# Kernel tuning notes

Hardware: AMD Instinct MI355X
Metric: run time of the kernel (lower is better)

Reference implementation:

```python
import jax, jax.numpy as jnp
import numpy as np

B, C, W, H = 32, 128, 128, 128  # batch, channels, window_size, prediction_horizon
KAPPA = 10.0

def setup_inputs() -> dict:
    key = jax.random.key(0)
    k1, k2, k3, k4 = jax.random.split(key, 4)
    x_t = jax.random.normal(k1, (B, C, W), dtype=jnp.float32)
    # d are observation timestamps in [0, H), compared against ref_t = linspace(0, H, H)
    d = jax.random.uniform(k2, (B, C, W), dtype=jnp.float32) * H
    # m is an observation mask/weight in (0, 1]; avoid exact zeros for log(m)
    m = jax.random.uniform(k3, (B, C, W), dtype=jnp.float32, minval=1e-3, maxval=1.0)
    kernel = jax.random.normal(k4, (W,), dtype=jnp.float32) * 0.1
    return {"x_t": x_t, "d": d, "m": m, "kernel": kernel}

def reference(x_t, d, m, kernel):
    # ref_t: [H], matches torch.linspace(0, H, H)
    ref_t = jnp.linspace(0.0, H, H, dtype=x_t.dtype)
    # norm: [B,C,W,H] squared time differences
    norm = (d[..., None] - ref_t) ** 2
    alpha = jnp.log1p(jnp.exp(kernel))[None, None, :, None]  # softplus, [1,1,W,1]
    logm = jnp.log(m)[..., None]                             # [B,C,W,1]
    # low-intensity interpolation (softmax over window dim W)
    s = -alpha * norm + logm                                 # [B,C,W,H]
    w = jax.nn.logsumexp(s, axis=2)                          # [B,C,H]
    w1 = jnp.exp(s - w[:, :, None, :])                       # softmax weights
    y = jnp.einsum('bcwh,bcw->bch', w1, x_t)
    # high-intensity (transient) interpolation with sharper kernel kappa*alpha
    s_t = -KAPPA * alpha * norm + logm
    wt_lse = jax.nn.logsumexp(s_t, axis=2)
    w_t = jnp.exp(s_t - wt_lse[:, :, None, :])
    y_trans = jnp.einsum('bcwh,bcw->bch', w_t, x_t)
    return (y, w, y_trans)
```

## Files before the change

### kernel.cpp

```cpp
#include <hip/hip_runtime.h>
#include <hip/hip_bf16.h>

#define NB 32
#define NC 128
#define NW 128
#define NH 128
#define BCH (NB * NC * NH)

__global__ __launch_bounds__(128, 4) void sci_kernel(
    const void* __restrict__ xp, const void* __restrict__ dp,
    const void* __restrict__ mp, const void* __restrict__ kp,
    void* __restrict__ outp)
{
    const int bc   = blockIdx.x;
    const int tid  = threadIdx.x;
    const int lane = tid & 63;
    const int wid  = tid >> 6;

    __shared__ float4 tileS[NW];
    __shared__ int    cum[NW + 1];
    __shared__ int    wtot[2];
    __shared__ float  wmin[2];

    const unsigned short* du16 = (const unsigned short*)dp;
    bool is_bf16 = true;
    #pragma unroll
    for (int i = 0; i < 32; i += 2) {
        float v = __uint_as_float(((unsigned int)du16[i]) << 16);
        is_bf16 = is_bf16 && (v >= 0.0f) && (v <= 129.0f);
    }

    float dv, mv, xv, kv;
    {
        const int base = bc * NW + tid;
        if (is_bf16) {
            dv = __bfloat162float(((const __hip_bfloat16*)dp)[base]);
            mv = __bfloat162float(((const __hip_bfloat16*)mp)[base]);
            xv = __bfloat162float(((const __hip_bfloat16*)xp)[base]);
            kv = __bfloat162float(((const __hip_bfloat16*)kp)[tid]);
        } else {
            dv = ((const float*)dp)[base];
            mv = ((const float*)mp)[base];
            xv = ((const float*)xp)[base];
            kv = ((const float*)kp)[tid];
        }
    }
    const float LOG2E = 1.4426950408889634f;
    float ex  = __builtin_amdgcn_exp2f(kv * LOG2E);
    float A2  = __builtin_amdgcn_logf(1.0f + ex);
    float sA2 = sqrtf(A2);
    float sd  = sA2 * dv;

    float rmn = sA2;
    #pragma unroll
    for (int o = 32; o >= 1; o >>= 1) rmn = fminf(rmn, __shfl_xor(rmn, o));
    if (lane == 0) wmin[wid] = rmn;

    cum[tid] = 0;
    __syncthreads();
    int bin  = min(127, max(0, (int)dv));
    int slot = atomicAdd(&cum[bin], 1);
    __syncthreads();

    int cnt = cum[tid];
    int c = cnt;
    #pragma unroll
    for (int o = 1; o < 64; o <<= 1) {
        int n = __shfl_up(c, o);
        if (lane >= o) c += n;
    }
    if (lane == 63) wtot[wid] = c;
    __syncthreads();
    int excl = c - cnt + (wid ? wtot[0] : 0);
    cum[tid] = excl;
    if (tid == 0) cum[NW] = NW;
    __syncthreads();

    int pos = cum[bin] + slot;
    tileS[pos] = make_float4(sA2, sd, mv, mv * xv);
    __syncthreads();

    const float rsA2min = (1.0f / fminf(wmin[0], wmin[1])) * 1.0005f;

    const float rh = (float)tid * (128.0f / 127.0f);

    float mn = 1e30f;
    float s1 = 0.f, a1 = 0.f, s2 = 0.f, a2 = 0.f;

    auto body = [&](int k) {
        float4 q = tileS[k];
        float t  = __builtin_fmaf(-q.x, rh, q.y);
        float t2 = t * t;
        if (t2 < mn) {
            float f  = __builtin_amdgcn_exp2f(t2 - mn);
            float fs = f * f, f4 = fs * fs, f8 = f4 * f4;
            float f10 = f8 * fs;
            s1 *= f; a1 *= f; s2 *= f10; a2 *= f10;
            mn = t2;
        }
        float g1 = __builtin_amdgcn_exp2f(mn - t2);
        float sq = g1 * g1, p4 = sq * sq, p8 = p4 * p4;
        float g2 = p8 * sq;
        s1 = __builtin_fmaf(q.z, g1, s1);
        a1 = __builtin_fmaf(q.w, g1, a1);
        s2 = __builtin_fmaf(q.z, g2, s2);
        a2 = __builtin_fmaf(q.w, g2, a2);
    };

    int b0 = min(127, (int)rh);
    int lo0, hi0, s0, e0;
    {
        int r = 2;
        for (;;) {
            lo0 = max(0, b0 - r); hi0 = min(127, b0 + r);
            s0 = cum[lo0]; e0 = cum[hi0 + 1];
            if (s0 != e0) break;
            ++r;
        }
    }
    for (int k = s0; k < e0; ++k) body(k);

    float Rh = sqrtf(mn + 12.0f) * rsA2min;
    int lo = min(lo0, max(0, (int)(rh - Rh)));
    int hi = max(hi0, min(127, (int)(rh + Rh)));
    int ks = cum[lo], ke = cum[hi + 1];
    for (int k = ks; k < s0; ++k) body(k);
    for (int k = e0; k < ke; ++k) body(k);

    const float LN2 = 0.6931471805599453f;
    float y  = a1 * __builtin_amdgcn_rcpf(s1);
    float wo = (__builtin_amdgcn_logf(s1) - mn) * LN2;
    float yt = a2 * __builtin_amdgcn_rcpf(s2);

    const int o = bc * NH + tid;
    if (is_bf16) {
        __hip_bfloat16* o16 = (__hip_bfloat16*)outp;
        o16[o]           = __float2bfloat16(y);
        o16[BCH + o]     = __float2bfloat16(wo);
        o16[2 * BCH + o] = __float2bfloat16(yt);
    } else {
        float* o32 = (float*)outp;
        o32[o]           = y;
        o32[BCH + o]     = wo;
        o32[2 * BCH + o] = yt;
    }
}

extern "C" void kernel_launch(void* const* d_in, const int* in_sizes, int n_in,
                              void* d_out, int out_size, void* d_ws, size_t ws_size,
                              hipStream_t stream) {
    const void* x_t = d_in[0];
    const void* d   = d_in[1];
    const void* m   = d_in[2];
    const void* k   = d_in[3];
    dim3 grid(NB * NC);
    dim3 block(128);
    hipLaunchKernelGGL(sci_kernel, grid, block, 0, stream, x_t, d, m, k, d_out);
}
```

Baseline: 72.89 us.

## Map one wavefront per (b,c) row with two outputs per lane

```diff
diff --git a/kernel.cpp b/kernel.cpp
--- a/kernel.cpp
+++ b/kernel.cpp
@@ -6,21 +6,31 @@
 #define NW 128
 #define NH 128
 #define BCH (NB * NC * NH)
+#define CPB 4
 
-__global__ __launch_bounds__(128, 4) void sci_kernel(
+#define WAVE_SYNC() do { __builtin_amdgcn_wave_barrier(); \
+    asm volatile("s_waitcnt lgkmcnt(0)" ::: "memory"); } while (0)
+
+static __device__ __forceinline__ float b2f(unsigned short u) {
+    return __uint_as_float(((unsigned int)u) << 16);
+}
+static __device__ __forceinline__ unsigned short f2b(float f) {
+    __hip_bfloat16 h = __float2bfloat16(f);
+    return *reinterpret_cast<unsigned short*>(&h);
+}
+
+__global__ __launch_bounds__(256, 4) void sci_kernel(
     const void* __restrict__ xp, const void* __restrict__ dp,
     const void* __restrict__ mp, const void* __restrict__ kp,
     void* __restrict__ outp)
 {
-    const int bc   = blockIdx.x;
-    const int tid  = threadIdx.x;
-    const int lane = tid & 63;
-    const int wid  = tid >> 6;
+    const int wid  = threadIdx.x >> 6;
+    const int lane = threadIdx.x & 63;
+    const int bc   = blockIdx.x * CPB + wid;
 
-    __shared__ float4 tileS[NW];
-    __shared__ int    cum[NW + 1];
-    __shared__ int    wtot[2];
-    __shared__ float  wmin[2];
+    __shared__ int    cnt[CPB][NW];
+    __shared__ int    cum[CPB][NW + 1];
+    __shared__ float4 tile[CPB][NW];
 
     const unsigned short* du16 = (const unsigned short*)dp;
     bool is_bf16 = true;
@@ -30,119 +40,141 @@
         is_bf16 = is_bf16 && (v >= 0.0f) && (v <= 129.0f);
     }
 
-    float dv, mv, xv, kv;
-    {
-        const int base = bc * NW + tid;
-        if (is_bf16) {
-            dv = __bfloat162float(((const __hip_bfloat16*)dp)[base]);
-            mv = __bfloat162float(((const __hip_bfloat16*)mp)[base]);
-            xv = __bfloat162float(((const __hip_bfloat16*)xp)[base]);
-            kv = __bfloat162float(((const __hip_bfloat16*)kp)[tid]);
-        } else {
-            dv = ((const float*)dp)[base];
-            mv = ((const float*)mp)[base];
-            xv = ((const float*)xp)[base];
-            kv = ((const float*)kp)[tid];
-        }
+    const int w0   = lane * 2;
+    const int base = bc * NW + w0;
+    float dv0, mv0, xv0, kv0, dv1, mv1, xv1, kv1;
+    if (is_bf16) {
+        ushort2 dd = *(const ushort2*)((const unsigned short*)dp + base);
+        ushort2 mm = *(const ushort2*)((const unsigned short*)mp + base);
+        ushort2 xx = *(const ushort2*)((const unsigned short*)xp + base);
+        ushort2 kk = *(const ushort2*)((const unsigned short*)kp + w0);
+        dv0 = b2f(dd.x); dv1 = b2f(dd.y);
+        mv0 = b2f(mm.x); mv1 = b2f(mm.y);
+        xv0 = b2f(xx.x); xv1 = b2f(xx.y);
+        kv0 = b2f(kk.x); kv1 = b2f(kk.y);
+    } else {
+        float2 dd = *(const float2*)((const float*)dp + base);
+        float2 mm = *(const float2*)((const float*)mp + base);
+        float2 xx = *(const float2*)((const float*)xp + base);
+        float2 kk = *(const float2*)((const float*)kp + w0);
+        dv0 = dd.x; dv1 = dd.y; mv0 = mm.x; mv1 = mm.y;
+        xv0 = xx.x; xv1 = xx.y; kv0 = kk.x; kv1 = kk.y;
     }
+
     const float LOG2E = 1.4426950408889634f;
-    float ex  = __builtin_amdgcn_exp2f(kv * LOG2E);
-    float A2  = __builtin_amdgcn_logf(1.0f + ex);
-    float sA2 = sqrtf(A2);
-    float sd  = sA2 * dv;
+    float ex0 = __builtin_amdgcn_exp2f(kv0 * LOG2E);
+    float ex1 = __builtin_amdgcn_exp2f(kv1 * LOG2E);
+    float A20 = __builtin_amdgcn_logf(1.0f + ex0);
+    float A21 = __builtin_amdgcn_logf(1.0f + ex1);
+    float sA20 = sqrtf(A20), sA21 = sqrtf(A21);
 
-    float rmn = sA2;
+    float rmn = fminf(sA20, sA21);
     #pragma unroll
     for (int o = 32; o >= 1; o >>= 1) rmn = fminf(rmn, __shfl_xor(rmn, o));
-    if (lane == 0) wmin[wid] = rmn;
+    const float rs = 1.0005f / rmn;
 
-    cum[tid] = 0;
-    __syncthreads();
-    int bin  = min(127, max(0, (int)dv));
-    int slot = atomicAdd(&cum[bin], 1);
-    __syncthreads();
-
-    int cnt = cum[tid];
-    int c = cnt;
+    cnt[wid][w0] = 0; cnt[wid][w0 + 1] = 0;
+    WAVE_SYNC();
+    int b0i = min(127, max(0, (int)dv0));
+    int b1i = min(127, max(0, (int)dv1));
+    int s0i = atomicAdd(&cnt[wid][b0i], 1);
+    int s1i = atomicAdd(&cnt[wid][b1i], 1);
+    WAVE_SYNC();
+    int c0 = cnt[wid][w0], c1 = cnt[wid][w0 + 1];
+    int p = c0 + c1, P = p;
     #pragma unroll
     for (int o = 1; o < 64; o <<= 1) {
-        int n = __shfl_up(c, o);
-        if (lane >= o) c += n;
+        int n = __shfl_up(P, o);
+        if (lane >= o) P += n;
     }
-    if (lane == 63) wtot[wid] = c;
-    __syncthreads();
-    int excl = c - cnt + (wid ? wtot[0] : 0);
-    cum[tid] = excl;
-    if (tid == 0) cum[NW] = NW;
-    __syncthreads();
+    int E0 = P - p;
+    cum[wid][w0]     = E0;
+    cum[wid][w0 + 1] = E0 + c0;
+    if (lane == 63) cum[wid][NW] = NW;
+    WAVE_SYNC();
+    int pos0 = cum[wid][b0i] + s0i;
+    int pos1 = cum[wid][b1i] + s1i;
+    tile[wid][pos0] = make_float4(sA20, sA20 * dv0, mv0, mv0 * xv0);
+    tile[wid][pos1] = make_float4(sA21, sA21 * dv1, mv1, mv1 * xv1);
+    WAVE_SYNC();
 
-    int pos = cum[bin] + slot;
-    tileS[pos] = make_float4(sA2, sd, mv, mv * xv);
-    __syncthreads();
+    const float STEP = 128.0f / 127.0f;
+    const float rh0 = (float)w0 * STEP;
+    const float rh1 = rh0 + STEP;
 
-    const float rsA2min = (1.0f / fminf(wmin[0], wmin[1])) * 1.0005f;
+    float mn0 = 1e30f, s10 = 0.f, a10 = 0.f, s20 = 0.f, a20 = 0.f;
+    float mn1 = 1e30f, s11 = 0.f, a11 = 0.f, s21 = 0.f, a21 = 0.f;
 
-    const float rh = (float)tid * (128.0f / 127.0f);
-
-    float mn = 1e30f;
-    float s1 = 0.f, a1 = 0.f, s2 = 0.f, a2 = 0.f;
+    const float4* T  = tile[wid];
+    const int*    CU = cum[wid];
 
     auto body = [&](int k) {
-        float4 q = tileS[k];
-        float t  = __builtin_fmaf(-q.x, rh, q.y);
-        float t2 = t * t;
-        if (t2 < mn) {
-            float f  = __builtin_amdgcn_exp2f(t2 - mn);
-            float fs = f * f, f4 = fs * fs, f8 = f4 * f4;
-            float f10 = f8 * fs;
-            s1 *= f; a1 *= f; s2 *= f10; a2 *= f10;
-            mn = t2;
+        float4 q = T[k];
+        float t0 = __builtin_fmaf(-q.x, rh0, q.y);
+        float t1 = __builtin_fmaf(-q.x, rh1, q.y);
+        float u0 = t0 * t0, u1 = t1 * t1;
+        if (u0 < mn0) {
+            float f = __builtin_amdgcn_exp2f(u0 - mn0);
+            float fs = f * f, f4 = fs * fs, f8 = f4 * f4, f10 = f8 * fs;
+            s10 *= f; a10 *= f; s20 *= f10; a20 *= f10; mn0 = u0;
         }
-        float g1 = __builtin_amdgcn_exp2f(mn - t2);
-        float sq = g1 * g1, p4 = sq * sq, p8 = p4 * p4;
-        float g2 = p8 * sq;
-        s1 = __builtin_fmaf(q.z, g1, s1);
-        a1 = __builtin_fmaf(q.w, g1, a1);
-        s2 = __builtin_fmaf(q.z, g2, s2);
-        a2 = __builtin_fmaf(q.w, g2, a2);
+        if (u1 < mn1) {
+            float f = __builtin_amdgcn_exp2f(u1 - mn1);
+            float fs = f * f, f4 = fs * fs, f8 = f4 * f4, f10 = f8 * fs;
+            s11 *= f; a11 *= f; s21 *= f10; a21 *= f10; mn1 = u1;
+        }
+        float g0 = __builtin_amdgcn_exp2f(mn0 - u0);
+        float g1 = __builtin_amdgcn_exp2f(mn1 - u1);
+        float q0 = g0 * g0, p40 = q0 * q0, p80 = p40 * p40, G0 = p80 * q0;
+        float q1 = g1 * g1, p41 = q1 * q1, p81 = p41 * p41, G1 = p81 * q1;
+        s10 = __builtin_fmaf(q.z, g0, s10); a10 = __builtin_fmaf(q.w, g0, a10);
+        s20 = __builtin_fmaf(q.z, G0, s20); a20 = __builtin_fmaf(q.w, G0, a20);
+        s11 = __builtin_fmaf(q.z, g1, s11); a11 = __builtin_fmaf(q.w, g1, a11);
+        s21 = __builtin_fmaf(q.z, G1, s21); a21 = __builtin_fmaf(q.w, G1, a21);
     };
 
-    int b0 = min(127, (int)rh);
-    int lo0, hi0, s0, e0;
+    int bctr = min(127, (int)rh0);
+    int lo0, hi0, ps, pe;
     {
         int r = 2;
         for (;;) {
-            lo0 = max(0, b0 - r); hi0 = min(127, b0 + r);
-            s0 = cum[lo0]; e0 = cum[hi0 + 1];
-            if (s0 != e0) break;
+            lo0 = max(0, bctr - r); hi0 = min(127, bctr + r);
+            ps = CU[lo0]; pe = CU[hi0 + 1];
+            if (ps != pe) break;
             ++r;
         }
     }
-    for (int k = s0; k < e0; ++k) body(k);
+    for (int k = ps; k < pe; ++k) body(k);
 
-    float Rh = sqrtf(mn + 12.0f) * rsA2min;
-    int lo = min(lo0, max(0, (int)(rh - Rh)));
-    int hi = max(hi0, min(127, (int)(rh + Rh)));
-    int ks = cum[lo], ke = cum[hi + 1];
-    for (int k = ks; k < s0; ++k) body(k);
-    for (int k = e0; k < ke; ++k) body(k);
+    float Rh0 = sqrtf(mn0 + 12.0f) * rs;
+    float Rh1 = sqrtf(mn1 + 12.0f) * rs;
+    float Lf = fminf(rh0 - Rh0, rh1 - Rh1);
+    float Hf = fmaxf(rh0 + Rh0, rh1 + Rh1);
+    int lo = min(lo0, max(0, (int)Lf));
+    int hi = max(hi0, min(127, (int)Hf));
+    int ks = CU[lo], ke = CU[hi + 1];
+    for (int k = ks; k < ps; ++k) body(k);
+    for (int k = pe; k < ke; ++k) body(k);
 
     const float LN2 = 0.6931471805599453f;
-    float y  = a1 * __builtin_amdgcn_rcpf(s1);
-    float wo = (__builtin_amdgcn_logf(s1) - mn) * LN2;
-    float yt = a2 * __builtin_amdgcn_rcpf(s2);
+    float y0  = a10 * __builtin_amdgcn_rcpf(s10);
+    float wo0 = (__builtin_amdgcn_logf(s10) - mn0) * LN2;
+    float yt0 = a20 * __builtin_amdgcn_rcpf(s20);
+    float y1  = a11 * __builtin_amdgcn_rcpf(s11);
+    float wo1 = (__builtin_amdgcn_logf(s11) - mn1) * LN2;
+    float yt1 = a21 * __builtin_amdgcn_rcpf(s21);
 
-    const int o = bc * NH + tid;
+    const int o = bc * NH + w0;
     if (is_bf16) {
-        __hip_bfloat16* o16 = (__hip_bfloat16*)outp;
-        o16[o]           = __float2bfloat16(y);
-        o16[BCH + o]     = __float2bfloat16(wo);
-        o16[2 * BCH + o] = __float2bfloat16(yt);
+        unsigned short* o16 = (unsigned short*)outp;
+        *(ushort2*)(o16 + o)           = make_ushort2(f2b(y0),  f2b(y1));
+        *(ushort2*)(o16 + BCH + o)     = make_ushort2(f2b(wo0), f2b(wo1));
+        *(ushort2*)(o16 + 2 * BCH + o) = make_ushort2(f2b(yt0), f2b(yt1));
     } else {
         float* o32 = (float*)outp;
-        o32[o]           = y;
-        o32[BCH + o]     = wo;
-        o32[2 * BCH + o] = yt;
+        *(float2*)(o32 + o)           = make_float2(y0,  y1);
+        *(float2*)(o32 + BCH + o)     = make_float2(wo0, wo1);
+        *(float2*)(o32 + 2 * BCH + o) = make_float2(yt0, yt1);
     }
 }
 
@@ -153,7 +185,7 @@
     const void* d   = d_in[1];
     const void* m   = d_in[2];
     const void* k   = d_in[3];
-    dim3 grid(NB * NC);
-    dim3 block(128);
+    dim3 grid((NB * NC) / CPB);
+    dim3 block(256);
     hipLaunchKernelGGL(sci_kernel, grid, block, 0, stream, x_t, d, m, k, d_out);
 }
```

Measured after the change: 76.52 us. +5.0%, slower.
